# Kernel tuning notes

Hardware: AMD Instinct MI355X
Metric: run time of the kernel (lower is better)

Reference implementation:

```python
import jax, jax.numpy as jnp
import numpy as np

D_MODEL = 512
NEG = -1e9


def setup_inputs() -> dict:
    key = jax.random.key(0)
    ks = jax.random.split(key, 8)
    B, S, D = 8, 2048, D_MODEL
    scale = 1.0 / np.sqrt(D)
    x = jax.random.normal(ks[0], (B, S, D), dtype=jnp.float32)
    event_lengths = jax.random.randint(ks[1], (B,), 1, S + 1)
    Wq = jax.random.normal(ks[2], (D, D), dtype=jnp.float32) * scale
    bq = jax.random.normal(ks[3], (D,), dtype=jnp.float32) * 0.01
    Wk = jax.random.normal(ks[4], (D, D), dtype=jnp.float32) * scale
    bk = jax.random.normal(ks[5], (D,), dtype=jnp.float32) * 0.01
    Wv = jax.random.normal(ks[6], (D, D), dtype=jnp.float32) * scale
    bv = jax.random.normal(ks[7], (D,), dtype=jnp.float32) * 0.01
    return {"x": x, "event_lengths": event_lengths, "Wq": Wq, "bq": bq,
            "Wk": Wk, "bk": bk, "Wv": Wv, "bv": bv}


def reference(x, event_lengths, Wq, bq, Wk, bk, Wv, bv):
    B, S, D = x.shape
    inv_scale = 1.0 / jnp.sqrt(jnp.float32(D))
    # torch nn.Linear: y = x @ W^T + b
    q = jnp.einsum('bsd,ed->bse', x, Wq) + bq
    k = jnp.einsum('bsd,ed->bse', x, Wk) + bk
    v = jnp.einsum('bsd,ed->bse', x, Wv) + bv
    scores = jnp.einsum('bqd,bkd->bqk', q, k) * inv_scale  # [B,S,S]
    idx = jnp.arange(S)
    L = event_lengths[:, None, None]  # [B,1,1]
    mask = (idx[None, :, None] < L) & (idx[None, None, :] < L)  # [B,S,S]
    scores = jnp.where(mask, scores, NEG)
    attn = jax.nn.softmax(scores, axis=-1)
    # dropout is identity at eval time
    return jnp.einsum('bqk,bkd->bqd', attn, v)
```

## Files before the change

### kernel.cpp

```cpp
#include <hip/hip_runtime.h>
#include <hip/hip_bf16.h>
#include <cstdint>

#define DEV static __device__ __forceinline__

typedef __attribute__((ext_vector_type(8))) short bf16x8;
typedef __attribute__((ext_vector_type(4))) float f32x4;
typedef __attribute__((ext_vector_type(4))) float float4v;
typedef __attribute__((ext_vector_type(8))) unsigned short us8;
typedef __attribute__((ext_vector_type(4))) unsigned short us4;

constexpr int SEQ = 2048;
constexpr int DM = 512;
constexpr float INV_SCALE = 0.044194173824159216f;
constexpr float LOG2E = 1.4426950408889634f;
constexpr float SEXP = INV_SCALE * LOG2E;

DEV unsigned short f2bf(float f) {
  unsigned int u = __float_as_uint(f);
  u = u + 0x7FFFu + ((u >> 16) & 1u);
  return (unsigned short)(u >> 16);
}
DEV float bf2f(unsigned short h) { return __uint_as_float(((unsigned int)h) << 16); }

DEV void gload_lds16(const void* g, void* l) {
  __builtin_amdgcn_global_load_lds(
      (const __attribute__((address_space(1))) void*)g,
      (__attribute__((address_space(3))) void*)l, 16, 0, 0);
}

__global__ void convert_x_kernel(const float* __restrict__ x, unsigned short* __restrict__ xb) {
  int64_t i = ((int64_t)blockIdx.x * 256 + threadIdx.x) * 8;
  float4v a = *(const float4v*)(x + i);
  float4v b = *(const float4v*)(x + i + 4);
  us8 o;
  o[0] = f2bf(a[0]); o[1] = f2bf(a[1]); o[2] = f2bf(a[2]); o[3] = f2bf(a[3]);
  o[4] = f2bf(b[0]); o[5] = f2bf(b[1]); o[6] = f2bf(b[2]); o[7] = f2bf(b[3]);
  *(us8*)(xb + i) = o;
}

__global__ void convert_w_kernel(const float* __restrict__ wq, const float* __restrict__ wk,
                                 const float* __restrict__ wv, unsigned short* __restrict__ wb) {
  int w = blockIdx.x >> 8;
  int blk = blockIdx.x & 255;
  const float* src = (w == 0) ? wq : ((w == 1) ? wk : wv);
  int i = (blk * 256 + (int)threadIdx.x) * 4;
  float4v a = *(const float4v*)(src + i);
  us4 o;
  o[0] = f2bf(a[0]); o[1] = f2bf(a[1]); o[2] = f2bf(a[2]); o[3] = f2bf(a[3]);
  *(us4*)(wb + (w << 18) + i) = o;
}

__global__ __launch_bounds__(256) void qkv_gemm_kernel(
    const unsigned short* __restrict__ xb, const unsigned short* __restrict__ wb,
    const float* __restrict__ bq, const float* __restrict__ bk, const float* __restrict__ bv,
    unsigned short* __restrict__ Qb, unsigned short* __restrict__ Kb,
    unsigned short* __restrict__ VTb)
{
  const int bid = blockIdx.x;
  const int eidx = bid >> 3;
  const int mrow = ((bid & 7) << 4) | (eidx & 15);
  const int wn = eidx >> 4;
  const int which = wn >> 2;
  const int m0 = mrow << 7;
  const int n0 = (wn & 3) << 7;
  const unsigned short* W = wb + ((int64_t)which << 18);
  const int tid = threadIdx.x;
  const int lane = tid & 63, wid = tid >> 6;
  const int lo = lane & 15, hi = lane >> 4;
  const int wrow = wid >> 1, wcol = wid & 1;

  __shared__ alignas(16) unsigned short lA[128 * 64];
  __shared__ alignas(16) unsigned short lB[128 * 64];

  f32x4 acc[4][4];
  #pragma unroll
  for (int i = 0; i < 4; ++i)
    #pragma unroll
    for (int j = 0; j < 4; ++j) acc[i][j] = (f32x4){0.f, 0.f, 0.f, 0.f};

  for (int k0 = 0; k0 < 512; k0 += 64) {
    if (k0) __syncthreads();
    #pragma unroll
    for (int i = 0; i < 4; ++i) {
      const int m = (i << 8) + tid;
      const int mw = (i << 8) + (wid << 6);
      const int row = m >> 3, c = m & 7;
      const int ca = c ^ (row & 7);
      gload_lds16(xb + ((int64_t)(m0 + row) << 9) + k0 + (ca << 3), lA + (mw << 3));
      gload_lds16(W  + ((int64_t)(n0 + row) << 9) + k0 + (ca << 3), lB + (mw << 3));
    }
    __syncthreads();

    #pragma unroll
    for (int ks = 0; ks < 2; ++ks) {
      bf16x8 af[4], bfr[4];
      #pragma unroll
      for (int mf = 0; mf < 4; ++mf) {
        const int row = (wrow << 6) + (mf << 4) + lo;
        const int cc = ((ks << 2) + hi) ^ (row & 7);
        af[mf] = *(const bf16x8*)(lA + (row << 6) + (cc << 3));
      }
      #pragma unroll
      for (int nf = 0; nf < 4; ++nf) {
        const int row = (wcol << 6) + (nf << 4) + lo;
        const int cc = ((ks << 2) + hi) ^ (row & 7);
        bfr[nf] = *(const bf16x8*)(lB + (row << 6) + (cc << 3));
      }
      #pragma unroll
      for (int mf = 0; mf < 4; ++mf)
        #pragma unroll
        for (int nf = 0; nf < 4; ++nf)
          acc[mf][nf] = __builtin_amdgcn_mfma_f32_16x16x32_bf16(af[mf], bfr[nf], acc[mf][nf], 0, 0, 0);
    }
  }

  const float* bias = (which == 0) ? bq : ((which == 1) ? bk : bv);
  if (which < 2) {
    unsigned short* outp = (which == 0) ? Qb : Kb;
    #pragma unroll
    for (int nf = 0; nf < 4; ++nf) {
      const int e = n0 + (wcol << 6) + (nf << 4) + lo;
      const float bb = bias[e];
      #pragma unroll
      for (int mf = 0; mf < 4; ++mf) {
        const int rowg = m0 + (wrow << 6) + (mf << 4) + (hi << 2);
        #pragma unroll
        for (int r = 0; r < 4; ++r)
          outp[((int64_t)(rowg + r) << 9) + e] = f2bf(acc[mf][nf][r] + bb);
      }
    }
  } else {
    #pragma unroll
    for (int nf = 0; nf < 4; ++nf) {
      const int e = n0 + (wcol << 6) + (nf << 4) + lo;
      const float bb = bias[e];
      #pragma unroll
      for (int mf = 0; mf < 4; ++mf) {
        const int rowg = m0 + (wrow << 6) + (mf << 4) + (hi << 2);
        const int bidx = rowg >> 11;
        const int s = rowg & 2047;
        us4 pk;
        pk[0] = f2bf(acc[mf][nf][0] + bb);
        pk[1] = f2bf(acc[mf][nf][1] + bb);
        pk[2] = f2bf(acc[mf][nf][2] + bb);
        pk[3] = f2bf(acc[mf][nf][3] + bb);
        *(us4*)(VTb + (((int64_t)(bidx << 9) + e) << 11) + s) = pk;
      }
    }
  }
}

__global__ void vmean_kernel(const unsigned short* __restrict__ VTb, float* __restrict__ vmean) {
  const int row = blockIdx.x;
  const unsigned short* src = VTb + (int64_t)row * SEQ;
  const int tid = threadIdx.x;
  us8 v = *(const us8*)(src + tid * 8);
  float s = 0.f;
  #pragma unroll
  for (int j = 0; j < 8; ++j) s += bf2f(v[j]);
  #pragma unroll
  for (int off = 1; off < 64; off <<= 1) s += __shfl_xor(s, off);
  __shared__ float ps[4];
  const int lane = tid & 63, wid = tid >> 6;
  if (lane == 0) ps[wid] = s;
  __syncthreads();
  if (tid == 0) vmean[row] = (ps[0] + ps[1] + ps[2] + ps[3]) * (1.f / 2048.f);
}

__global__ __launch_bounds__(256) void score_gemm_kernel(
    const unsigned short* __restrict__ Qb, const unsigned short* __restrict__ Kb,
    const int* __restrict__ ev, unsigned short* __restrict__ P, int b0)
{
  const int z = blockIdx.z;
  const int b = b0 + z;
  const int L = ev[b];
  const int q0 = blockIdx.x << 7;
  const int k0g = blockIdx.y << 7;
  if (q0 >= L || k0g >= L) return;

  const unsigned short* Qrows = Qb + ((int64_t)b << 20);
  const unsigned short* Krows = Kb + ((int64_t)b << 20);
  const int tid = threadIdx.x;
  const int lane = tid & 63, wid = tid >> 6;
  const int lo = lane & 15, hi = lane >> 4;
  const int wrow = wid >> 1, wcol = wid & 1;

  __shared__ alignas(16) unsigned short lA[128 * 64];
  __shared__ alignas(16) unsigned short lB[128 * 64];

  f32x4 acc[4][4];
  #pragma unroll
  for (int i = 0; i < 4; ++i)
    #pragma unroll
    for (int j = 0; j < 4; ++j) acc[i][j] = (f32x4){0.f, 0.f, 0.f, 0.f};

  for (int k0 = 0; k0 < 512; k0 += 64) {
    if (k0) __syncthreads();
    #pragma unroll
    for (int i = 0; i < 4; ++i) {
      const int m = (i << 8) + tid;
      const int mw = (i << 8) + (wid << 6);
      const int row = m >> 3, c = m & 7;
      const int ca = c ^ (row & 7);
      gload_lds16(Qrows + ((int64_t)(q0 + row) << 9) + k0 + (ca << 3), lA + (mw << 3));
      gload_lds16(Krows + ((int64_t)(k0g + row) << 9) + k0 + (ca << 3), lB + (mw << 3));
    }
    __syncthreads();

    #pragma unroll
    for (int ks = 0; ks < 2; ++ks) {
      bf16x8 af[4], bfr[4];
      #pragma unroll
      for (int mf = 0; mf < 4; ++mf) {
        const int row = (wrow << 6) + (mf << 4) + lo;
        const int cc = ((ks << 2) + hi) ^ (row & 7);
        af[mf] = *(const bf16x8*)(lA + (row << 6) + (cc << 3));
      }
      #pragma unroll
      for (int nf = 0; nf < 4; ++nf) {
        const int row = (wcol << 6) + (nf << 4) + lo;
        const int cc = ((ks << 2) + hi) ^ (row & 7);
        bfr[nf] = *(const bf16x8*)(lB + (row << 6) + (cc << 3));
      }
      #pragma unroll
      for (int mf = 0; mf < 4; ++mf)
        #pragma unroll
        for (int nf = 0; nf < 4; ++nf)
          acc[mf][nf] = __builtin_amdgcn_mfma_f32_16x16x32_bf16(af[mf], bfr[nf], acc[mf][nf], 0, 0, 0);
    }
  }

  unsigned short* Pz = P + ((int64_t)z << 22);
  #pragma unroll
  for (int nf = 0; nf < 4; ++nf) {
    const int kcol = k0g + (wcol << 6) + (nf << 4) + lo;
    const bool kok = kcol < L;
    #pragma unroll
    for (int mf = 0; mf < 4; ++mf) {
      const int rowg = q0 + (wrow << 6) + (mf << 4) + (hi << 2);
      #pragma unroll
      for (int r = 0; r < 4; ++r) {
        const float p = (kok && (rowg + r < L)) ? exp2f(acc[mf][nf][r] * SEXP) : 0.f;
        Pz[((int64_t)(rowg + r) << 11) + kcol] = f2bf(p);
      }
    }
  }
}

__global__ __launch_bounds__(256) void pv_gemm_kernel(
    const unsigned short* __restrict__ P, const unsigned short* __restrict__ VTb,
    const float* __restrict__ vmean, const int* __restrict__ ev,
    float* __restrict__ out, int b0)
{
  const int z = blockIdx.z;
  const int b = b0 + z;
  const int L = ev[b];
  const int q0 = blockIdx.x << 7;
  const int d0 = blockIdx.y << 7;
  const int tid = threadIdx.x;

  float* outb = out + ((int64_t)b << 20);
  const float* vm = vmean + (b << 9);

  if (q0 >= L) {
    #pragma unroll
    for (int j = 0; j < 16; ++j) {
      const int r = (tid >> 5) + (j << 3);
      const int c = (tid & 31) << 2;
      *(float4v*)(outb + ((int64_t)(q0 + r) << 9) + d0 + c) = *(const float4v*)(vm + d0 + c);
    }
    return;
  }

  const int lane = tid & 63, wid = tid >> 6;
  const int lo = lane & 15, hi = lane >> 4;
  const int wrow = wid >> 1, wcol = wid & 1;

  __shared__ alignas(16) unsigned short lA[128 * 64];
  __shared__ alignas(16) unsigned short lB[128 * 64];
  __shared__ float lpart[128][4];

  const unsigned short* Pz = P + ((int64_t)z << 22);
  const unsigned short* Vrows = VTb + ((int64_t)(b << 9) << 11);

  f32x4 acc[4][4];
  #pragma unroll
  for (int i = 0; i < 4; ++i)
    #pragma unroll
    for (int j = 0; j < 4; ++j) acc[i][j] = (f32x4){0.f, 0.f, 0.f, 0.f};
  float ls[4] = {0.f, 0.f, 0.f, 0.f};

  const int nk = (L + 63) >> 6;
  for (int kk = 0; kk < nk; ++kk) {
    if (kk) __syncthreads();
    #pragma unroll
    for (int i = 0; i < 4; ++i) {
      const int m = (i << 8) + tid;
      const int mw = (i << 8) + (wid << 6);
      const int row = m >> 3, c = m & 7;
      const int ca = c ^ (row & 7);
      gload_lds16(Pz + ((int64_t)(q0 + row) << 11) + (kk << 6) + (ca << 3), lA + (mw << 3));
      gload_lds16(Vrows + ((int64_t)(d0 + row) << 11) + (kk << 6) + (ca << 3), lB + (mw << 3));
    }
    __syncthreads();

    #pragma unroll
    for (int ks = 0; ks < 2; ++ks) {
      bf16x8 af[4], bfr[4];
      #pragma unroll
      for (int mf = 0; mf < 4; ++mf) {
        const int row = (wrow << 6) + (mf << 4) + lo;
        const int cc = ((ks << 2) + hi) ^ (row & 7);
        af[mf] = *(const bf16x8*)(lA + (row << 6) + (cc << 3));
      }
      #pragma unroll
      for (int nf = 0; nf < 4; ++nf) {
        const int row = (wcol << 6) + (nf << 4) + lo;
        const int cc = ((ks << 2) + hi) ^ (row & 7);
        bfr[nf] = *(const bf16x8*)(lB + (row << 6) + (cc << 3));
      }
      if (wcol == 0) {
        #pragma unroll
        for (int mf = 0; mf < 4; ++mf) {
          float t = 0.f;
          #pragma unroll
          for (int j = 0; j < 8; ++j) t += bf2f((unsigned short)af[mf][j]);
          ls[mf] += t;
        }
      }
      #pragma unroll
      for (int mf = 0; mf < 4; ++mf)
        #pragma unroll
        for (int nf = 0; nf < 4; ++nf)
          acc[mf][nf] = __builtin_amdgcn_mfma_f32_16x16x32_bf16(af[mf], bfr[nf], acc[mf][nf], 0, 0, 0);
    }
  }

  if (wcol == 0) {
    #pragma unroll
    for (int mf = 0; mf < 4; ++mf)
      lpart[(wrow << 6) + (mf << 4) + lo][hi] = ls[mf];
  }
  __syncthreads();

  #pragma unroll
  for (int mf = 0; mf < 4; ++mf) {
    const int rowb = (wrow << 6) + (mf << 4) + (hi << 2);
    float rl[4];
    #pragma unroll
    for (int r = 0; r < 4; ++r) {
      const float l = lpart[rowb + r][0] + lpart[rowb + r][1] +
                      lpart[rowb + r][2] + lpart[rowb + r][3];
      rl[r] = 1.0f / l;
    }
    #pragma unroll
    for (int nf = 0; nf < 4; ++nf) {
      const int col = d0 + (wcol << 6) + (nf << 4) + lo;
      const float vmc = vm[col];
      #pragma unroll
      for (int r = 0; r < 4; ++r) {
        const int rowg = q0 + rowb + r;
        const float val = (rowg < L) ? (acc[mf][nf][r] * rl[r]) : vmc;
        outb[((int64_t)rowg << 9) + col] = val;
      }
    }
  }
}

extern "C" void kernel_launch(void* const* d_in, const int* in_sizes, int n_in,
                              void* d_out, int out_size, void* d_ws, size_t ws_size,
                              hipStream_t stream) {
  const float* x  = (const float*)d_in[0];
  const int* ev   = (const int*)d_in[1];
  const float* Wq = (const float*)d_in[2];
  const float* bq = (const float*)d_in[3];
  const float* Wk = (const float*)d_in[4];
  const float* bk = (const float*)d_in[5];
  const float* Wv = (const float*)d_in[6];
  const float* bv = (const float*)d_in[7];
  float* out = (float*)d_out;

  unsigned short* xb  = (unsigned short*)d_ws;
  unsigned short* wb  = xb + (int64_t)16384 * 512;
  unsigned short* Qb  = wb + 3 * 512 * 512;
  unsigned short* Kb  = Qb + (int64_t)16384 * 512;
  unsigned short* VTb = Kb + (int64_t)16384 * 512;
  float* vmean = (float*)(VTb + (int64_t)16384 * 512);
  unsigned short* Ptail = (unsigned short*)(vmean + 8 * 512);

  const size_t base_bytes = (size_t)((char*)Ptail - (char*)d_ws);
  const size_t pbytes = (size_t)SEQ * SEQ * 2;
  int nb;
  unsigned short* P;
  if (ws_size >= base_bytes + 8 * pbytes)      { nb = 8; P = Ptail; }
  else if (ws_size >= base_bytes + 4 * pbytes) { nb = 4; P = Ptail; }
  else                                         { nb = 2; P = xb; }

  convert_x_kernel<<<4096, 256, 0, stream>>>(x, xb);
  convert_w_kernel<<<768, 256, 0, stream>>>(Wq, Wk, Wv, wb);
  qkv_gemm_kernel<<<1536, 256, 0, stream>>>(xb, wb, bq, bk, bv, Qb, Kb, VTb);
  vmean_kernel<<<4096, 256, 0, stream>>>(VTb, vmean);

  for (int c = 0; c < 8 / nb; ++c) {
    score_gemm_kernel<<<dim3(16, 16, nb), 256, 0, stream>>>(Qb, Kb, ev, P, c * nb);
    pv_gemm_kernel<<<dim3(16, 4, nb), 256, 0, stream>>>(P, VTb, vmean, ev, out, c * nb);
  }
}
```

Measured before the change: 123.7 us.

## Halve PV GEMM query tile and double-buffer LDS loads

The P·V kernel moves from 128-row to 64-row query tiles, doubling the grid to 32x4 blocks so more blocks are resident and fewer rows in each tile sit past the sequence length. It also double-buffers the LDS tiles, issuing the next K-step's global-to-LDS loads before the MFMA work on the current buffer, which hides load latency and removes one barrier per iteration. The cost is more LDS per block, re-reading the V tile twice as often across blocks, and smaller per-wave MFMA tiles that lower compute density.

```diff
diff --git a/kernel.cpp b/kernel.cpp
--- a/kernel.cpp
+++ b/kernel.cpp
@@ -256,7 +256,7 @@
   const int z = blockIdx.z;
   const int b = b0 + z;
   const int L = ev[b];
-  const int q0 = blockIdx.x << 7;
+  const int q0 = blockIdx.x << 6;
   const int d0 = blockIdx.y << 7;
   const int tid = threadIdx.x;
 
@@ -265,9 +265,9 @@
 
   if (q0 >= L) {
     #pragma unroll
-    for (int j = 0; j < 16; ++j) {
-      const int r = (tid >> 5) + (j << 3);
-      const int c = (tid & 31) << 2;
+    for (int j = 0; j < 8; ++j) {
+      const int idx = tid + (j << 8);
+      const int r = idx >> 5, c = (idx & 31) << 2;
       *(float4v*)(outb + ((int64_t)(q0 + r) << 9) + d0 + c) = *(const float4v*)(vm + d0 + c);
     }
     return;
@@ -277,52 +277,68 @@
   const int lo = lane & 15, hi = lane >> 4;
   const int wrow = wid >> 1, wcol = wid & 1;
 
-  __shared__ alignas(16) unsigned short lA[128 * 64];
-  __shared__ alignas(16) unsigned short lB[128 * 64];
-  __shared__ float lpart[128][4];
+  __shared__ alignas(16) unsigned short lA[2][64 * 64];
+  __shared__ alignas(16) unsigned short lB[2][128 * 64];
+  __shared__ float lpart[64][4];
 
   const unsigned short* Pz = P + ((int64_t)z << 22);
   const unsigned short* Vrows = VTb + ((int64_t)(b << 9) << 11);
 
-  f32x4 acc[4][4];
-  #pragma unroll
-  for (int i = 0; i < 4; ++i)
+  f32x4 acc[2][4];
+  #pragma unroll
+  for (int i = 0; i < 2; ++i)
     #pragma unroll
     for (int j = 0; j < 4; ++j) acc[i][j] = (f32x4){0.f, 0.f, 0.f, 0.f};
-  float ls[4] = {0.f, 0.f, 0.f, 0.f};
+  float ls[2] = {0.f, 0.f};
 
   const int nk = (L + 63) >> 6;
-  for (int kk = 0; kk < nk; ++kk) {
-    if (kk) __syncthreads();
+
+  auto stage = [&](int cur, int kk) {
+    #pragma unroll
+    for (int i = 0; i < 2; ++i) {
+      const int m = (i << 8) + tid;
+      const int mw = (i << 8) + (wid << 6);
+      const int row = m >> 3, c = m & 7;
+      const int ca = c ^ (row & 7);
+      gload_lds16(Pz + ((int64_t)(q0 + row) << 11) + (kk << 6) + (ca << 3),
+                  &lA[cur][mw << 3]);
+    }
     #pragma unroll
     for (int i = 0; i < 4; ++i) {
       const int m = (i << 8) + tid;
       const int mw = (i << 8) + (wid << 6);
       const int row = m >> 3, c = m & 7;
       const int ca = c ^ (row & 7);
-      gload_lds16(Pz + ((int64_t)(q0 + row) << 11) + (kk << 6) + (ca << 3), lA + (mw << 3));
-      gload_lds16(Vrows + ((int64_t)(d0 + row) << 11) + (kk << 6) + (ca << 3), lB + (mw << 3));
-    }
-    __syncthreads();
+      gload_lds16(Vrows + ((int64_t)(d0 + row) << 11) + (kk << 6) + (ca << 3),
+                  &lB[cur][mw << 3]);
+    }
+  };
+
+  stage(0, 0);
+  __syncthreads();
+  int cur = 0;
+
+  for (int kk = 0; kk < nk; ++kk) {
+    if (kk + 1 < nk) stage(cur ^ 1, kk + 1);
 
     #pragma unroll
     for (int ks = 0; ks < 2; ++ks) {
-      bf16x8 af[4], bfr[4];
-      #pragma unroll
-      for (int mf = 0; mf < 4; ++mf) {
-        const int row = (wrow << 6) + (mf << 4) + lo;
-        const int cc = ((ks << 2) + hi) ^ (row & 7);
-        af[mf] = *(const bf16x8*)(lA + (row << 6) + (cc << 3));
+      bf16x8 af[2], bfr[4];
+      #pragma unroll
+      for (int mf = 0; mf < 2; ++mf) {
+        const int row = (wrow << 5) + (mf << 4) + lo;
+        const int cc = ((ks << 2) + hi) ^ (row & 7);
+        af[mf] = *(const bf16x8*)(&lA[cur][(row << 6) + (cc << 3)]);
       }
       #pragma unroll
       for (int nf = 0; nf < 4; ++nf) {
         const int row = (wcol << 6) + (nf << 4) + lo;
         const int cc = ((ks << 2) + hi) ^ (row & 7);
-        bfr[nf] = *(const bf16x8*)(lB + (row << 6) + (cc << 3));
+        bfr[nf] = *(const bf16x8*)(&lB[cur][(row << 6) + (cc << 3)]);
       }
       if (wcol == 0) {
         #pragma unroll
-        for (int mf = 0; mf < 4; ++mf) {
+        for (int mf = 0; mf < 2; ++mf) {
           float t = 0.f;
           #pragma unroll
           for (int j = 0; j < 8; ++j) t += bf2f((unsigned short)af[mf][j]);
@@ -330,23 +346,26 @@
         }
       }
       #pragma unroll
-      for (int mf = 0; mf < 4; ++mf)
+      for (int mf = 0; mf < 2; ++mf)
         #pragma unroll
         for (int nf = 0; nf < 4; ++nf)
           acc[mf][nf] = __builtin_amdgcn_mfma_f32_16x16x32_bf16(af[mf], bfr[nf], acc[mf][nf], 0, 0, 0);
     }
+
+    __syncthreads();
+    cur ^= 1;
   }
 
   if (wcol == 0) {
     #pragma unroll
-    for (int mf = 0; mf < 4; ++mf)
-      lpart[(wrow << 6) + (mf << 4) + lo][hi] = ls[mf];
+    for (int mf = 0; mf < 2; ++mf)
+      lpart[(wrow << 5) + (mf << 4) + lo][hi] = ls[mf];
   }
   __syncthreads();
 
   #pragma unroll
-  for (int mf = 0; mf < 4; ++mf) {
-    const int rowb = (wrow << 6) + (mf << 4) + (hi << 2);
+  for (int mf = 0; mf < 2; ++mf) {
+    const int rowb = (wrow << 5) + (mf << 4) + (hi << 2);
     float rl[4];
     #pragma unroll
     for (int r = 0; r < 4; ++r) {
@@ -404,6 +423,6 @@
 
   for (int c = 0; c < 8 / nb; ++c) {
     score_gemm_kernel<<<dim3(16, 16, nb), 256, 0, stream>>>(Qb, Kb, ev, P, c * nb);
-    pv_gemm_kernel<<<dim3(16, 4, nb), 256, 0, stream>>>(P, VTb, vmean, ev, out, c * nb);
-  }
-}
+    pv_gemm_kernel<<<dim3(32, 4, nb), 256, 0, stream>>>(P, VTb, vmean, ev, out, c * nb);
+  }
+}
```

After: 120.9 us. 2.2% less time.
